# Performance work log

Measured on AMD Instinct MI355X. Metric: run time of the kernel, lower is better.

The kernel has to match this reference:

```python
import jax
import jax.numpy as jnp
from jax import lax
import numpy as np

# ---- static RPN config (mirrors init_kwargs) ----
STRIDES = (8, 16)
SIZES = ((32, 32), (16, 16))
SCALES = ((64.0 ** 2,), (128.0 ** 2,))
RATIOS = ((0.5, 1.0, 2.0), (0.5, 1.0, 2.0))
IMAGE_SIZE = (256, 256)
NMS_THRESH = 0.7
POST_NMS_TOP_N = 2000
NUM_LEVELS = 2
TOP_K_PER_LEVEL = POST_NMS_TOP_N // NUM_LEVELS  # padded NMS output slots per level


def _generate_anchors(stride, scales, ratios, size, image_size):
    """Anchors of shape (H*W*A, 4) in (x1,y1,x2,y2), clamped to image."""
    H, W = size
    cy = (np.arange(H, dtype=np.float32) + 0.5) * stride
    cx = (np.arange(W, dtype=np.float32) + 0.5) * stride
    ws, hs = [], []
    for s in scales:
        for r in ratios:
            ws.append(np.sqrt(s / r))
            hs.append(np.sqrt(s * r))
    ws = np.asarray(ws, np.float32)  # [A]
    hs = np.asarray(hs, np.float32)
    cxg, cyg = np.meshgrid(cx, cy)  # [H, W]
    x1 = cxg[..., None] - 0.5 * ws
    y1 = cyg[..., None] - 0.5 * hs
    x2 = cxg[..., None] + 0.5 * ws
    y2 = cyg[..., None] + 0.5 * hs
    a = np.stack([x1, y1, x2, y2], axis=-1)  # [H, W, A, 4]
    a[..., 0] = np.clip(a[..., 0], 0, image_size[0])
    a[..., 1] = np.clip(a[..., 1], 0, image_size[1])
    a[..., 2] = np.clip(a[..., 2], 0, image_size[0])
    a[..., 3] = np.clip(a[..., 3], 0, image_size[1])
    return a.reshape(-1, 4).astype(np.float32)


ANCHORS = [
    _generate_anchors(STRIDES[i], SCALES[i], RATIOS[i], SIZES[i], IMAGE_SIZE)
    for i in range(NUM_LEVELS)
]


def conv2d(x, w, b, padding):
    y = lax.conv_general_dilated(
        x, w, window_strides=(1, 1), padding=padding,
        dimension_numbers=("NCHW", "OIHW", "NCHW"))
    return y + b[None, :, None, None]


def decode_boxes(anchors, deltas):
    """Standard R-CNN box decode. anchors [N,4], deltas [..., N, 4]."""
    wa = anchors[:, 2] - anchors[:, 0]
    ha = anchors[:, 3] - anchors[:, 1]
    cxa = anchors[:, 0] + 0.5 * wa
    cya = anchors[:, 1] + 0.5 * ha
    dx, dy, dw, dh = deltas[..., 0], deltas[..., 1], deltas[..., 2], deltas[..., 3]
    cx = dx * wa + cxa
    cy = dy * ha + cya
    w = jnp.exp(dw) * wa
    h = jnp.exp(dh) * ha
    return jnp.stack([cx - 0.5 * w, cy - 0.5 * h, cx + 0.5 * w, cy + 0.5 * h], axis=-1)


def clamp_boxes(b):
    return jnp.stack([
        jnp.clip(b[..., 0], 0.0, IMAGE_SIZE[0]),
        jnp.clip(b[..., 1], 0.0, IMAGE_SIZE[1]),
        jnp.clip(b[..., 2], 0.0, IMAGE_SIZE[0]),
        jnp.clip(b[..., 3], 0.0, IMAGE_SIZE[1]),
    ], axis=-1)


def _pairwise_iou(b):
    # b: [N, 4] -> [N, N] IoU (torchvision convention, no +1)
    area = (b[:, 2] - b[:, 0]) * (b[:, 3] - b[:, 1])
    lt = jnp.maximum(b[:, None, :2], b[None, :, :2])
    rb = jnp.minimum(b[:, None, 2:], b[None, :, 2:])
    wh = jnp.clip(rb - lt, 0.0)
    inter = wh[..., 0] * wh[..., 1]
    return inter / (area[:, None] + area[None, :] - inter)


def nms_padded(boxes, scores, thresh, top_k):
    """Exact greedy NMS; returns (top_k,4) boxes and (top_k,) scores padded with -1."""
    N = boxes.shape[0]
    order = jnp.argsort(-scores)
    b = boxes[order]
    s = scores[order]
    iou = _pairwise_iou(b)  # [N, N]

    def body(supp, xs):
        row, i = xs
        keep_i = jnp.logical_not(supp[i])
        supp = supp | (keep_i & (row > thresh) & (jnp.arange(N) > i))
        return supp, keep_i

    _, keep = lax.scan(body, jnp.zeros((N,), bool), (iou, jnp.arange(N)))
    rank = jnp.cumsum(keep) - 1  # position among kept, in score order
    slot = jnp.where(keep & (rank < top_k), rank, top_k)  # overflow -> dump row
    out_b = jnp.full((top_k + 1, 4), -1.0, boxes.dtype).at[slot].set(b)
    out_s = jnp.full((top_k + 1,), -1.0, scores.dtype).at[slot].set(s)
    return out_b[:top_k], out_s[:top_k]


def _rpn_level(feat, anchors, conv_w, conv_b, cls_w, cls_b, reg_w, reg_b):
    x = jax.nn.relu(conv2d(feat, conv_w, conv_b, "SAME"))
    cls = conv2d(x, cls_w, cls_b, "VALID")              # [BS, A, H, W]
    reg = conv2d(x, reg_w, reg_b, "VALID")              # [BS, 4A, H, W]
    BS, A, H, W = cls.shape
    cls = cls.transpose(0, 2, 3, 1).reshape(BS, -1)                      # [BS, HWA]
    reg = reg.transpose(0, 2, 3, 1).reshape(BS, H, W, A, 4).reshape(BS, -1, 4)
    boxes = clamp_boxes(decode_boxes(anchors, lax.stop_gradient(reg)))   # [BS, HWA, 4]
    scores = jax.nn.sigmoid(lax.stop_gradient(cls))                      # [BS, HWA]
    kb, ks = jax.vmap(lambda bb, ss: nms_padded(bb, ss, NMS_THRESH, TOP_K_PER_LEVEL))(boxes, scores)
    return kb, ks


def setup_inputs() -> dict:
    key = jax.random.key(0)
    ks = jax.random.split(key, 5)
    C = 256
    A = 3
    return {
        "feat0": jax.random.normal(ks[0], (4, C, 32, 32), jnp.float32),
        "feat1": jax.random.normal(ks[1], (4, C, 16, 16), jnp.float32),
        "conv_w": 0.01 * jax.random.normal(ks[2], (C, C, 3, 3), jnp.float32),
        "conv_b": jnp.zeros((C,), jnp.float32),
        "cls_w": 0.01 * jax.random.normal(ks[3], (A, C, 1, 1), jnp.float32),
        "cls_b": jnp.zeros((A,), jnp.float32),
        "reg_w": 0.01 * jax.random.normal(ks[4], (4 * A, C, 1, 1), jnp.float32),
        "reg_b": jnp.zeros((4 * A,), jnp.float32),
    }


def reference(feat0, feat1, conv_w, conv_b, cls_w, cls_b, reg_w, reg_b):
    feats = [feat0, feat1]
    kb_all, ks_all = [], []
    for i in range(NUM_LEVELS):
        kb, ks = _rpn_level(feats[i], jnp.asarray(ANCHORS[i]),
                            conv_w, conv_b, cls_w, cls_b, reg_w, reg_b)
        kb_all.append(kb)
        ks_all.append(ks)
    bboxes = jnp.concatenate(kb_all, axis=1)   # [BS, POST_NMS_TOP_N, 4]
    scores = jnp.concatenate(ks_all, axis=1)   # [BS, POST_NMS_TOP_N]
    idx = jnp.argsort(-scores, axis=1)         # descending; -1 pads go last
    bboxes = jnp.take_along_axis(bboxes, idx[..., None], axis=1)
    return bboxes
```

## Files before the change

kernel.cpp:

```cpp
#include <hip/hip_runtime.h>
#include <math.h>


typedef double d4 __attribute__((ext_vector_type(4)));

__global__ __launch_bounds__(256, 4) void conv3_sk_u(
    const float* __restrict__ feat0, const float* __restrict__ feat1,
    const float* __restrict__ conv_w,
    double* __restrict__ part0, double* __restrict__ part1)
{
  __shared__ float Ald[2][16][72];
  __shared__ float Bld[2][16][72];
  const int t = threadIdx.x;
  const int bid = blockIdx.x;
  const float* feat;
  double* part;
  int oc_t, p_t, k_base, hw_sh, w_sh, H;
  if (bid < 1024) {
    int kc = bid >> 8;
    feat = feat0; part = part0 + (size_t)kc * 4096 * 256;
    oc_t = bid & 3; p_t = (bid >> 2) & 63;
    k_base = kc * 576; hw_sh = 10; w_sh = 5; H = 32;
  } else {
    int b2 = bid - 1024;
    int kc = b2 >> 6;
    feat = feat1; part = part1 + (size_t)kc * 1024 * 256;
    oc_t = b2 & 3; p_t = (b2 >> 2) & 15;
    k_base = kc * 576; hw_sh = 8; w_sh = 4; H = 16;
  }
  const int oc_base = oc_t * 64;
  const int p_base  = p_t * 64;
  const int wmask = H - 1, hwmask = (1 << hw_sh) - 1;
  const int skk = t >> 4;
  const int q4  = (t & 15) * 4;

  float a_r[4], b_r[4];
  auto load_tile = [&](int kt) {
    const int k0 = k_base + kt * 16;
    const float* wrow = conv_w + (size_t)(oc_base + q4) * 2304 + (k0 + skk);
#pragma unroll
    for (int u = 0; u < 4; ++u) a_r[u] = wrow[(size_t)u * 2304];
    int p = p_base + q4;
    int b = p >> hw_sh, pin = p & hwmask;
    int y = pin >> w_sh, x0 = pin & wmask;
    int k = k0 + skk;
    int ic = k / 9, rr = k - ic * 9;
    int ky = rr / 3, kx = rr - ky * 3;
    int iy = y + ky - 1;
    const float* frow = feat + (((b << 8) + ic) << hw_sh) + (iy << w_sh);
    bool yok = (unsigned)iy < (unsigned)H;
#pragma unroll
    for (int u = 0; u < 4; ++u) {
      int ix = x0 + u + kx - 1;
      b_r[u] = (yok && (unsigned)ix < (unsigned)H) ? frow[ix] : 0.f;
    }
  };

  const int lane = t & 63;
  const int wv = t >> 6;
  const int wo = (wv >> 1) << 5;
  const int wp = (wv & 1) << 5;
  const int lr = lane >> 4;
  const int lc = lane & 15;

  int rowm[4], colm[4];
  {
    d4 pz = {0.0, 0.0, 0.0, 0.0};
    double pa1 = (lr == 0) ? (double)(lc + 1) : 0.0;
    double pb1 = (lr == 0) ? 1.0 : 0.0;
    d4 prow = __builtin_amdgcn_mfma_f64_16x16x4f64(pa1, pb1, pz, 0, 0, 0);
    double pa2 = (lr == 0) ? 1.0 : 0.0;
    double pb2 = (lr == 0) ? (double)(lc + 1) : 0.0;
    d4 pcol = __builtin_amdgcn_mfma_f64_16x16x4f64(pa2, pb2, pz, 0, 0, 0);
#pragma unroll
    for (int d = 0; d < 4; ++d) {
      rowm[d] = ((int)prow[d] - 1) & 15;
      colm[d] = ((int)pcol[d] - 1) & 15;
    }
  }

  d4 acc00 = {0.0, 0.0, 0.0, 0.0};
  d4 acc01 = {0.0, 0.0, 0.0, 0.0};
  d4 acc10 = {0.0, 0.0, 0.0, 0.0};
  d4 acc11 = {0.0, 0.0, 0.0, 0.0};

  load_tile(0);
  for (int kt = 0; kt < 36; ++kt) {
    const int buf = kt & 1;
    *(float4*)&Ald[buf][skk][q4] = make_float4(a_r[0], a_r[1], a_r[2], a_r[3]);
    *(float4*)&Bld[buf][skk][q4] = make_float4(b_r[0], b_r[1], b_r[2], b_r[3]);
    __syncthreads();
    if (kt + 1 < 36) load_tile(kt + 1);
#pragma unroll
    for (int kc = 0; kc < 4; ++kc) {
      const int kr = (kc << 2) + lr;
      double a0 = (double)Ald[buf][kr][wo + lc];
      double a1 = (double)Ald[buf][kr][wo + 16 + lc];
      double b0 = (double)Bld[buf][kr][wp + lc];
      double b1 = (double)Bld[buf][kr][wp + 16 + lc];
      acc00 = __builtin_amdgcn_mfma_f64_16x16x4f64(a0, b0, acc00, 0, 0, 0);
      acc01 = __builtin_amdgcn_mfma_f64_16x16x4f64(a0, b1, acc01, 0, 0, 0);
      acc10 = __builtin_amdgcn_mfma_f64_16x16x4f64(a1, b0, acc10, 0, 0, 0);
      acc11 = __builtin_amdgcn_mfma_f64_16x16x4f64(a1, b1, acc11, 0, 0, 0);
    }
  }

  {
    const int p00 = p_base + wp;
    const int oc00 = oc_base + wo;
#pragma unroll
    for (int d = 0; d < 4; ++d) {
      const int rm = rowm[d], cm = colm[d];
      part[(size_t)(p00 + cm)      * 256 + (oc00 + rm)]      = acc00[d];
      part[(size_t)(p00 + 16 + cm) * 256 + (oc00 + rm)]      = acc01[d];
      part[(size_t)(p00 + cm)      * 256 + (oc00 + 16 + rm)] = acc10[d];
      part[(size_t)(p00 + 16 + cm) * 256 + (oc00 + 16 + rm)] = acc11[d];
    }
  }
}

__global__ __launch_bounds__(256) void rhd_k(
    const double* __restrict__ part0, const double* __restrict__ part1,
    const float* __restrict__ conv_b,
    const float* __restrict__ cls_w, const float* __restrict__ cls_b,
    const float* __restrict__ reg_w, const float* __restrict__ reg_b,
    float* __restrict__ box0, float* __restrict__ sc0,
    float* __restrict__ box1, float* __restrict__ sc1)
{
  int wid = (blockIdx.x * 256 + threadIdx.x) >> 6;
  int lane = threadIdx.x & 63;
  int lvl = wid >= 4096;
  const double* part = lvl ? part1 : part0;
  int p = lvl ? wid - 4096 : wid;
  int M = lvl ? 1024 : 4096;
  double s4[4];
  {
    float4 bv = ((const float4*)conv_b)[lane];
    s4[0] = (double)bv.x; s4[1] = (double)bv.y;
    s4[2] = (double)bv.z; s4[3] = (double)bv.w;
  }
#pragma unroll
  for (int ks = 0; ks < 4; ++ks) {
    const double2* pr = (const double2*)(part + (size_t)ks * M * 256 + (size_t)p * 256);
    double2 a = pr[2 * lane], b = pr[2 * lane + 1];
    s4[0] += a.x; s4[1] += a.y; s4[2] += b.x; s4[3] += b.y;
  }
  float xv[4];
#pragma unroll
  for (int q = 0; q < 4; ++q) {
    float f = (float)s4[q];
    xv[q] = f > 0.f ? f : 0.f;
  }
  double acc[15];
#pragma unroll
  for (int o = 0; o < 15; ++o) {
    const float* wr = (o < 3) ? (cls_w + o * 256) : (reg_w + (o - 3) * 256);
    float4 wv = ((const float4*)wr)[lane];
    acc[o] = (double)wv.x * (double)xv[0] + (double)wv.y * (double)xv[1] +
             (double)wv.z * (double)xv[2] + (double)wv.w * (double)xv[3];
  }
#pragma unroll
  for (int d = 1; d < 64; d <<= 1)
#pragma unroll
    for (int o = 0; o < 15; ++o)
      acc[o] += __shfl_xor(acc[o], d, 64);
  if (lane < 3) {
    int a = lane;
    float cls = (float)(acc[a] + (double)cls_b[a]);
    float score = 1.f / (1.f + expf(-cls));
    float dx = (float)(acc[3 + a * 4 + 0] + (double)reg_b[a * 4 + 0]);
    float dy = (float)(acc[3 + a * 4 + 1] + (double)reg_b[a * 4 + 1]);
    float dw = (float)(acc[3 + a * 4 + 2] + (double)reg_b[a * 4 + 2]);
    float dh = (float)(acc[3 + a * 4 + 3] + (double)reg_b[a * 4 + 3]);
    int hw_sh = lvl ? 8 : 10, w_sh = lvl ? 4 : 5, Wd = lvl ? 16 : 32;
    float S = lvl ? 16.f : 8.f;
    double scale = lvl ? 16384.0 : 4096.0;
    int b = p >> hw_sh, pin = p & ((1 << hw_sh) - 1);
    int y = pin >> w_sh, x = pin & (Wd - 1);
    double ratio = (a == 0) ? 0.5 : (a == 1 ? 1.0 : 2.0);
    float w_a = (float)sqrt(scale / ratio);
    float h_a = (float)sqrt(scale * ratio);
    float cx = ((float)x + 0.5f) * S;
    float cy = ((float)y + 0.5f) * S;
    float x1 = cx - 0.5f * w_a, y1 = cy - 0.5f * h_a;
    float x2 = cx + 0.5f * w_a, y2 = cy + 0.5f * h_a;
    x1 = fminf(fmaxf(x1, 0.f), 256.f); y1 = fminf(fmaxf(y1, 0.f), 256.f);
    x2 = fminf(fmaxf(x2, 0.f), 256.f); y2 = fminf(fmaxf(y2, 0.f), 256.f);
    float wa = x2 - x1, ha = y2 - y1;
    float cxa = x1 + 0.5f * wa, cya = y1 + 0.5f * ha;
    float ncx = dx * wa + cxa;
    float ncy = dy * ha + cya;
    float nw = expf(dw) * wa;
    float nh = expf(dh) * ha;
    float bx1 = ncx - 0.5f * nw, by1 = ncy - 0.5f * nh;
    float bx2 = ncx + 0.5f * nw, by2 = ncy + 0.5f * nh;
    bx1 = fminf(fmaxf(bx1, 0.f), 256.f); by1 = fminf(fmaxf(by1, 0.f), 256.f);
    bx2 = fminf(fmaxf(bx2, 0.f), 256.f); by2 = fminf(fmaxf(by2, 0.f), 256.f);
    int n = pin * 3 + a;
    if (lvl) {
      ((float4*)box1)[(size_t)b * 768 + n] = make_float4(bx1, by1, bx2, by2);
      sc1[b * 768 + n] = score;
    } else {
      ((float4*)box0)[(size_t)b * 3072 + n] = make_float4(bx1, by1, bx2, by2);
      sc0[b * 3072 + n] = score;
    }
  }
}

__global__ __launch_bounds__(256) void sort_level_k(
    const float* __restrict__ sc0, const float* __restrict__ box0,
    float* __restrict__ ssc0, float* __restrict__ sbox0,
    const float* __restrict__ sc1, const float* __restrict__ box1,
    float* __restrict__ ssc1, float* __restrict__ sbox1)
{
  __shared__ __align__(16) float s[3072];
  int z = blockIdx.x;
  const float *sc, *box; float *ssc, *sbox; int N, b, c;
  if (z < 48) { sc = sc0; box = box0; ssc = ssc0; sbox = sbox0; N = 3072; b = z / 12; c = z % 12; }
  else { int z2 = z - 48; sc = sc1; box = box1; ssc = ssc1; sbox = sbox1; N = 768; b = z2 / 3; c = z2 % 3; }
  const float* scb = sc + (size_t)b * N;
  for (int j = threadIdx.x; j < N; j += 256) s[j] = scb[j];
  __syncthreads();
  int i = c * 256 + threadIdx.x;
  float si = s[i];
  int rank = 0;
  const float4* sv = (const float4*)s;
  for (int j4 = 0; j4 < (N >> 2); ++j4) {
    float4 v = sv[j4];
    int j = j4 * 4;
    rank += (v.x > si) || (v.x == si && (j + 0) < i);
    rank += (v.y > si) || (v.y == si && (j + 1) < i);
    rank += (v.z > si) || (v.z == si && (j + 2) < i);
    rank += (v.w > si) || (v.w == si && (j + 3) < i);
  }
  ssc[(size_t)b * N + rank] = si;
  float4 bi = ((const float4*)box)[(size_t)b * N + i];
  ((float4*)sbox)[(size_t)b * N + rank] = bi;
}

__global__ __launch_bounds__(256) void mask_col_k(
    const float* __restrict__ sbox0, const float* __restrict__ sbox1,
    unsigned long long* __restrict__ mask0, unsigned long long* __restrict__ mask1,
    unsigned long long* __restrict__ colD0, unsigned long long* __restrict__ colD1)
{
  int bid = blockIdx.x;
  if (bid < 2448) {
    __shared__ float4 bj[64];
    const float* sbox; unsigned long long* mask; int N, words, w, i_ch, b;
    if (bid < 2304) {
      sbox = sbox0; mask = mask0; N = 3072; words = 48;
      w = bid % 48; int r = bid / 48; i_ch = r % 12; b = r / 12;
    } else {
      int z = bid - 2304;
      sbox = sbox1; mask = mask1; N = 768; words = 12;
      w = z % 12; int r = z / 12; i_ch = r % 3; b = r / 3;
    }
    int i = i_ch * 256 + threadIdx.x;
    if (threadIdx.x < 64)
      bj[threadIdx.x] = ((const float4*)sbox)[(size_t)b * N + w * 64 + threadIdx.x];
    __syncthreads();
    float4 bi = ((const float4*)sbox)[(size_t)b * N + i];
    float ai = (bi.z - bi.x) * (bi.w - bi.y);
    unsigned long long m = 0ull;
#pragma unroll 16
    for (int jj = 0; jj < 64; ++jj) {
      int j = w * 64 + jj;
      float4 bv = bj[jj];
      float lx = fmaxf(bi.x, bv.x), ly = fmaxf(bi.y, bv.y);
      float rx = fminf(bi.z, bv.z), ry = fminf(bi.w, bv.w);
      float iw = fmaxf(rx - lx, 0.f), ih = fmaxf(ry - ly, 0.f);
      float inter = iw * ih;
      float aj = (bv.z - bv.x) * (bv.w - bv.y);
      float iou = inter / (ai + aj - inter);
      if ((iou > 0.7f) & (j > i)) m |= (1ull << jj);
    }
    mask[((size_t)b * N + i) * words + w] = m;
  } else {
    __shared__ float4 tb[4][64];
    int sub = threadIdx.x >> 6, lane = threadIdx.x & 63;
    const float* sbox; unsigned long long* colD; int N, tile, b;
    if (bid < 2496) {
      int unit = (bid - 2448) * 4 + sub;
      sbox = sbox0; colD = colD0; N = 3072;
      tile = unit % 48; b = unit / 48;
    } else {
      int unit = (bid - 2496) * 4 + sub;
      sbox = sbox1; colD = colD1; N = 768;
      tile = unit % 12; b = unit / 12;
    }
    tb[sub][lane] = ((const float4*)sbox)[(size_t)b * N + tile * 64 + lane];
    __syncthreads();
    float4 bq = tb[sub][lane];
    float aq = (bq.z - bq.x) * (bq.w - bq.y);
    unsigned long long col = 0ull;
#pragma unroll 16
    for (int ii = 0; ii < 64; ++ii) {
      float4 bi = tb[sub][ii];
      float lx = fmaxf(bq.x, bi.x), ly = fmaxf(bq.y, bi.y);
      float rx = fminf(bq.z, bi.z), ry = fminf(bq.w, bi.w);
      float iw = fmaxf(rx - lx, 0.f), ih = fmaxf(ry - ly, 0.f);
      float inter = iw * ih;
      float ai = (bi.z - bi.x) * (bi.w - bi.y);
      float iou = inter / (aq + ai - inter);
      if ((iou > 0.7f) & (lane > ii)) col |= (1ull << ii);
    }
    colD[(size_t)b * N + tile * 64 + lane] = col;
  }
}

__global__ __launch_bounds__(256) void nms_scan_k(
    const float* __restrict__ ssc0, const float* __restrict__ sbox0,
    const unsigned long long* __restrict__ mask0,
    const unsigned long long* __restrict__ colD0,
    const float* __restrict__ ssc1, const float* __restrict__ sbox1,
    const unsigned long long* __restrict__ mask1,
    const unsigned long long* __restrict__ colD1,
    float* __restrict__ cb, float* __restrict__ cs)
{
  int z = blockIdx.x;
  int lvl = z >> 2, b = z & 3;
  int N = lvl ? 768 : 3072;
  int words = lvl ? 12 : 48;
  const float* ssc = (lvl ? ssc1 : ssc0) + (size_t)b * N;
  const float4* sbox = ((const float4*)(lvl ? sbox1 : sbox0)) + (size_t)b * N;
  const unsigned long long* mask = (lvl ? mask1 : mask0) + (size_t)b * N * words;
  const unsigned long long* colD = (lvl ? colD1 : colD0) + (size_t)b * N;
  const int tid = threadIdx.x;
  const int lane = tid & 63;
  const int wv = tid >> 6;
  float* csb = cs + (size_t)b * 2000 + lvl * 1000;
  float4* cbb = (float4*)(cb + ((size_t)b * 2000 + lvl * 1000) * 4);

  __shared__ unsigned long long rem[48];
  __shared__ unsigned long long part[4][64];
  __shared__ unsigned long long keepSh;
  __shared__ int doneSh;

  if (tid < 48) rem[tid] = 0ull;
  if (tid == 0) doneSh = 0;
  for (int q = tid; q < 1000; q += 256) {
    csb[q] = -1.f;
    cbb[q] = make_float4(-1.f, -1.f, -1.f, -1.f);
  }
  unsigned long long colv = 0ull; float sc_i = 0.f; float4 bx_i;
  if (wv == 0) { colv = colD[lane]; sc_i = ssc[lane]; bx_i = sbox[lane]; }
  int kept_base = 0;
  __syncthreads();

  for (int t = 0; t < words; ++t) {
    unsigned long long v[16];
    if (lane < words) {
      const unsigned long long* rowb =
          mask + ((size_t)t * 64 + wv * 16) * words + lane;
#pragma unroll
      for (int s = 0; s < 16; ++s) v[s] = rowb[(size_t)s * words];
    }
    if (wv == 0) {
      unsigned long long wr = rem[t];
      bool rm = (wr >> lane) & 1ull;
      bool kp = false;
      unsigned long long Rv = wr;
      unsigned long long Kv = 0ull;
      while (true) {
        bool F = (!rm) && (!kp) && ((colv & ~Rv) == 0ull);
        unsigned long long Fv = __ballot(F);
        if (Fv == 0ull) break;
        kp = kp || F;
        Kv |= Fv;
        bool newr = (!rm) && (!kp) && ((colv & Fv) != 0ull);
        rm = rm || newr;
        Rv = __ballot(rm);
      }
      if (kp) {
        int rank = kept_base + __popcll(Kv & ((1ull << lane) - 1ull));
        if (rank < 1000) { csb[rank] = sc_i; cbb[rank] = bx_i; }
      }
      kept_base += __popcll(Kv);
      if (lane == 0) {
        keepSh = Kv;
        doneSh = (kept_base >= 1000 || t + 1 >= words) ? 1 : 0;
      }
      if (t + 1 < words) {
        int i2 = (t + 1) * 64 + lane;
        colv = colD[i2]; sc_i = ssc[i2]; bx_i = sbox[i2];
      }
    }
    __syncthreads();
    unsigned long long k64 = keepSh;
    int done = doneSh;
    if (lane < words) {
      unsigned long long acc = 0ull;
#pragma unroll
      for (int s = 0; s < 16; ++s)
        acc |= (((k64 >> (wv * 16 + s)) & 1ull) ? v[s] : 0ull);
      part[wv][lane] = acc;
    }
    __syncthreads();
    if (done) break;
    if (tid > t && tid < words)
      rem[tid] |= part[0][tid] | part[1][tid] | part[2][tid] | part[3][tid];
    __syncthreads();
  }
}

__global__ __launch_bounds__(256) void final_sort_k(
    const float* __restrict__ cs, const float* __restrict__ cb,
    float* __restrict__ out)
{
  __shared__ __align__(16) float s[2000];
  int b = blockIdx.x >> 3, c = blockIdx.x & 7;
  const float* csb = cs + (size_t)b * 2000;
  for (int j = threadIdx.x; j < 2000; j += 256) s[j] = csb[j];
  __syncthreads();
  if (threadIdx.x >= 250) return;
  int li = c * 250 + threadIdx.x;
  float si = s[li];
  int rank = 0;
  const float4* sv = (const float4*)s;
  for (int j4 = 0; j4 < 500; ++j4) {
    float4 v = sv[j4];
    int j = j4 * 4;
    rank += (v.x > si) || (v.x == si && (j + 0) < li);
    rank += (v.y > si) || (v.y == si && (j + 1) < li);
    rank += (v.z > si) || (v.z == si && (j + 2) < li);
    rank += (v.w > si) || (v.w == si && (j + 3) < li);
  }
  float4 bi = ((const float4*)cb)[(size_t)b * 2000 + li];
  ((float4*)out)[(size_t)b * 2000 + rank] = bi;
}

extern "C" void kernel_launch(void* const* d_in, const int* in_sizes, int n_in,
                              void* d_out, int out_size, void* d_ws, size_t ws_size,
                              hipStream_t stream) {
  const float* feat0  = (const float*)d_in[0];
  const float* feat1  = (const float*)d_in[1];
  const float* conv_w = (const float*)d_in[2];
  const float* conv_b = (const float*)d_in[3];
  const float* cls_w  = (const float*)d_in[4];
  const float* cls_b  = (const float*)d_in[5];
  const float* reg_w  = (const float*)d_in[6];
  const float* reg_b  = (const float*)d_in[7];

  char* p = (char*)d_ws;
  auto alloc = [&](size_t bytes) {
    char* r = p;
    p += (bytes + 255) & ~(size_t)255;
    return r;
  };
  double* part0 = (double*)alloc((size_t)4 * 4096 * 256 * 8);
  double* part1 = (double*)alloc((size_t)4 * 1024 * 256 * 8);
  float* box0 = (float*)alloc((size_t)4 * 3072 * 16);
  float* sc0  = (float*)alloc((size_t)4 * 3072 * 4);
  float* box1 = (float*)alloc((size_t)4 * 768 * 16);
  float* sc1  = (float*)alloc((size_t)4 * 768 * 4);
  float* sbox0 = (float*)alloc((size_t)4 * 3072 * 16);
  float* ssc0  = (float*)alloc((size_t)4 * 3072 * 4);
  float* sbox1 = (float*)alloc((size_t)4 * 768 * 16);
  float* ssc1  = (float*)alloc((size_t)4 * 768 * 4);
  unsigned long long* mask0 = (unsigned long long*)alloc((size_t)4 * 3072 * 48 * 8);
  unsigned long long* mask1 = (unsigned long long*)alloc((size_t)4 * 768 * 12 * 8);
  unsigned long long* colD0 = (unsigned long long*)alloc((size_t)4 * 3072 * 8);
  unsigned long long* colD1 = (unsigned long long*)alloc((size_t)4 * 768 * 8);
  float* cb = (float*)alloc((size_t)4 * 2000 * 16);
  float* cs = (float*)alloc((size_t)4 * 2000 * 4);

  conv3_sk_u<<<1280, 256, 0, stream>>>(feat0, feat1, conv_w, part0, part1);
  rhd_k<<<1280, 256, 0, stream>>>(part0, part1, conv_b, cls_w, cls_b,
                                  reg_w, reg_b, box0, sc0, box1, sc1);
  sort_level_k<<<60, 256, 0, stream>>>(sc0, box0, ssc0, sbox0,
                                       sc1, box1, ssc1, sbox1);
  mask_col_k<<<2508, 256, 0, stream>>>(sbox0, sbox1, mask0, mask1, colD0, colD1);
  nms_scan_k<<<8, 256, 0, stream>>>(ssc0, sbox0, mask0, colD0,
                                    ssc1, sbox1, mask1, colD1, cb, cs);
  final_sort_k<<<32, 256, 0, stream>>>(cs, cb, (float*)d_out);
}
```

Baseline: 467.7 us.

## Fuse post-conv stages into one persistent kernel with grid-wide soft barriers

Replaces the five post-convolution kernels (head decode, per-level sort, IoU mask build, NMS scan, final sort) with a single persistent kernel of 512 blocks. The stages are separated by software grid barriers that use atomic counters, and a memset clears the counters before each run. The goal is to remove per-launch overhead and the gaps between the small, serial stages. The risks are deadlock if all 512 blocks are not co-resident, and the cost of spinning on the global atomics.

After: 674.4 us. 44.2% more time.

```diff
diff --git a/kernel.cpp b/kernel.cpp
--- a/kernel.cpp
+++ b/kernel.cpp
@@ -119,314 +119,322 @@
   }
 }
 
-__global__ __launch_bounds__(256) void rhd_k(
+__device__ __forceinline__ void soft_barrier(unsigned int* bar, int idx) {
+  __syncthreads();
+  if (threadIdx.x == 0) {
+    __threadfence();
+    atomicAdd(&bar[idx], 1u);
+    while (atomicAdd(&bar[idx], 0u) < 512u)
+      __builtin_amdgcn_s_sleep(8);
+    __threadfence();
+  }
+  __syncthreads();
+}
+
+__global__ __launch_bounds__(256, 4) void fused_post_k(
     const double* __restrict__ part0, const double* __restrict__ part1,
     const float* __restrict__ conv_b,
     const float* __restrict__ cls_w, const float* __restrict__ cls_b,
     const float* __restrict__ reg_w, const float* __restrict__ reg_b,
     float* __restrict__ box0, float* __restrict__ sc0,
-    float* __restrict__ box1, float* __restrict__ sc1)
+    float* __restrict__ box1, float* __restrict__ sc1,
+    float* __restrict__ sbox0, float* __restrict__ ssc0,
+    float* __restrict__ sbox1, float* __restrict__ ssc1,
+    unsigned long long* __restrict__ mask0, unsigned long long* __restrict__ mask1,
+    unsigned long long* __restrict__ colD0, unsigned long long* __restrict__ colD1,
+    float* __restrict__ cb, float* __restrict__ cs,
+    float* __restrict__ out, unsigned int* bar)
 {
-  int wid = (blockIdx.x * 256 + threadIdx.x) >> 6;
-  int lane = threadIdx.x & 63;
-  int lvl = wid >= 4096;
-  const double* part = lvl ? part1 : part0;
-  int p = lvl ? wid - 4096 : wid;
-  int M = lvl ? 1024 : 4096;
-  double s4[4];
-  {
-    float4 bv = ((const float4*)conv_b)[lane];
-    s4[0] = (double)bv.x; s4[1] = (double)bv.y;
-    s4[2] = (double)bv.z; s4[3] = (double)bv.w;
-  }
-#pragma unroll
-  for (int ks = 0; ks < 4; ++ks) {
-    const double2* pr = (const double2*)(part + (size_t)ks * M * 256 + (size_t)p * 256);
-    double2 a = pr[2 * lane], b = pr[2 * lane + 1];
-    s4[0] += a.x; s4[1] += a.y; s4[2] += b.x; s4[3] += b.y;
-  }
-  float xv[4];
-#pragma unroll
-  for (int q = 0; q < 4; ++q) {
-    float f = (float)s4[q];
-    xv[q] = f > 0.f ? f : 0.f;
-  }
-  double acc[15];
-#pragma unroll
-  for (int o = 0; o < 15; ++o) {
-    const float* wr = (o < 3) ? (cls_w + o * 256) : (reg_w + (o - 3) * 256);
-    float4 wv = ((const float4*)wr)[lane];
-    acc[o] = (double)wv.x * (double)xv[0] + (double)wv.y * (double)xv[1] +
-             (double)wv.z * (double)xv[2] + (double)wv.w * (double)xv[3];
-  }
-#pragma unroll
-  for (int d = 1; d < 64; d <<= 1)
-#pragma unroll
-    for (int o = 0; o < 15; ++o)
-      acc[o] += __shfl_xor(acc[o], d, 64);
-  if (lane < 3) {
-    int a = lane;
-    float cls = (float)(acc[a] + (double)cls_b[a]);
-    float score = 1.f / (1.f + expf(-cls));
-    float dx = (float)(acc[3 + a * 4 + 0] + (double)reg_b[a * 4 + 0]);
-    float dy = (float)(acc[3 + a * 4 + 1] + (double)reg_b[a * 4 + 1]);
-    float dw = (float)(acc[3 + a * 4 + 2] + (double)reg_b[a * 4 + 2]);
-    float dh = (float)(acc[3 + a * 4 + 3] + (double)reg_b[a * 4 + 3]);
-    int hw_sh = lvl ? 8 : 10, w_sh = lvl ? 4 : 5, Wd = lvl ? 16 : 32;
-    float S = lvl ? 16.f : 8.f;
-    double scale = lvl ? 16384.0 : 4096.0;
-    int b = p >> hw_sh, pin = p & ((1 << hw_sh) - 1);
-    int y = pin >> w_sh, x = pin & (Wd - 1);
-    double ratio = (a == 0) ? 0.5 : (a == 1 ? 1.0 : 2.0);
-    float w_a = (float)sqrt(scale / ratio);
-    float h_a = (float)sqrt(scale * ratio);
-    float cx = ((float)x + 0.5f) * S;
-    float cy = ((float)y + 0.5f) * S;
-    float x1 = cx - 0.5f * w_a, y1 = cy - 0.5f * h_a;
-    float x2 = cx + 0.5f * w_a, y2 = cy + 0.5f * h_a;
-    x1 = fminf(fmaxf(x1, 0.f), 256.f); y1 = fminf(fmaxf(y1, 0.f), 256.f);
-    x2 = fminf(fmaxf(x2, 0.f), 256.f); y2 = fminf(fmaxf(y2, 0.f), 256.f);
-    float wa = x2 - x1, ha = y2 - y1;
-    float cxa = x1 + 0.5f * wa, cya = y1 + 0.5f * ha;
-    float ncx = dx * wa + cxa;
-    float ncy = dy * ha + cya;
-    float nw = expf(dw) * wa;
-    float nh = expf(dh) * ha;
-    float bx1 = ncx - 0.5f * nw, by1 = ncy - 0.5f * nh;
-    float bx2 = ncx + 0.5f * nw, by2 = ncy + 0.5f * nh;
-    bx1 = fminf(fmaxf(bx1, 0.f), 256.f); by1 = fminf(fmaxf(by1, 0.f), 256.f);
-    bx2 = fminf(fmaxf(bx2, 0.f), 256.f); by2 = fminf(fmaxf(by2, 0.f), 256.f);
-    int n = pin * 3 + a;
-    if (lvl) {
-      ((float4*)box1)[(size_t)b * 768 + n] = make_float4(bx1, by1, bx2, by2);
-      sc1[b * 768 + n] = score;
+  __shared__ __align__(16) char smem[12288];
+  const int t = threadIdx.x;
+
+  for (int u = blockIdx.x; u < 1280; u += 512) {
+    int wid = (u * 256 + t) >> 6;
+    int lane = t & 63;
+    int lvl = wid >= 4096;
+    const double* part = lvl ? part1 : part0;
+    int p = lvl ? wid - 4096 : wid;
+    int M = lvl ? 1024 : 4096;
+    double s4[4];
+    {
+      float4 bv = ((const float4*)conv_b)[lane];
+      s4[0] = (double)bv.x; s4[1] = (double)bv.y;
+      s4[2] = (double)bv.z; s4[3] = (double)bv.w;
+    }
+#pragma unroll
+    for (int ks = 0; ks < 4; ++ks) {
+      const double2* pr = (const double2*)(part + (size_t)ks * M * 256 + (size_t)p * 256);
+      double2 a = pr[2 * lane], b = pr[2 * lane + 1];
+      s4[0] += a.x; s4[1] += a.y; s4[2] += b.x; s4[3] += b.y;
+    }
+    float xv[4];
+#pragma unroll
+    for (int q = 0; q < 4; ++q) {
+      float f = (float)s4[q];
+      xv[q] = f > 0.f ? f : 0.f;
+    }
+    double acc[15];
+#pragma unroll
+    for (int o = 0; o < 15; ++o) {
+      const float* wr = (o < 3) ? (cls_w + o * 256) : (reg_w + (o - 3) * 256);
+      float4 wv = ((const float4*)wr)[lane];
+      acc[o] = (double)wv.x * (double)xv[0] + (double)wv.y * (double)xv[1] +
+               (double)wv.z * (double)xv[2] + (double)wv.w * (double)xv[3];
+    }
+#pragma unroll
+    for (int d = 1; d < 64; d <<= 1)
+#pragma unroll
+      for (int o = 0; o < 15; ++o)
+        acc[o] += __shfl_xor(acc[o], d, 64);
+    if (lane < 3) {
+      int a = lane;
+      float cls = (float)(acc[a] + (double)cls_b[a]);
+      float score = 1.f / (1.f + expf(-cls));
+      float dx = (float)(acc[3 + a * 4 + 0] + (double)reg_b[a * 4 + 0]);
+      float dy = (float)(acc[3 + a * 4 + 1] + (double)reg_b[a * 4 + 1]);
+      float dw = (float)(acc[3 + a * 4 + 2] + (double)reg_b[a * 4 + 2]);
+      float dh = (float)(acc[3 + a * 4 + 3] + (double)reg_b[a * 4 + 3]);
+      int hw_sh = lvl ? 8 : 10, w_sh = lvl ? 4 : 5, Wd = lvl ? 16 : 32;
+      float S = lvl ? 16.f : 8.f;
+      double scale = lvl ? 16384.0 : 4096.0;
+      int b = p >> hw_sh, pin = p & ((1 << hw_sh) - 1);
+      int y = pin >> w_sh, x = pin & (Wd - 1);
+      double ratio = (a == 0) ? 0.5 : (a == 1 ? 1.0 : 2.0);
+      float w_a = (float)sqrt(scale / ratio);
+      float h_a = (float)sqrt(scale * ratio);
+      float cx = ((float)x + 0.5f) * S;
+      float cy = ((float)y + 0.5f) * S;
+      float x1 = cx - 0.5f * w_a, y1 = cy - 0.5f * h_a;
+      float x2 = cx + 0.5f * w_a, y2 = cy + 0.5f * h_a;
+      x1 = fminf(fmaxf(x1, 0.f), 256.f); y1 = fminf(fmaxf(y1, 0.f), 256.f);
+      x2 = fminf(fmaxf(x2, 0.f), 256.f); y2 = fminf(fmaxf(y2, 0.f), 256.f);
+      float wa = x2 - x1, ha = y2 - y1;
+      float cxa = x1 + 0.5f * wa, cya = y1 + 0.5f * ha;
+      float ncx = dx * wa + cxa;
+      float ncy = dy * ha + cya;
+      float nw = expf(dw) * wa;
+      float nh = expf(dh) * ha;
+      float bx1 = ncx - 0.5f * nw, by1 = ncy - 0.5f * nh;
+      float bx2 = ncx + 0.5f * nw, by2 = ncy + 0.5f * nh;
+      bx1 = fminf(fmaxf(bx1, 0.f), 256.f); by1 = fminf(fmaxf(by1, 0.f), 256.f);
+      bx2 = fminf(fmaxf(bx2, 0.f), 256.f); by2 = fminf(fmaxf(by2, 0.f), 256.f);
+      int n = pin * 3 + a;
+      if (lvl) {
+        ((float4*)box1)[(size_t)b * 768 + n] = make_float4(bx1, by1, bx2, by2);
+        sc1[b * 768 + n] = score;
+      } else {
+        ((float4*)box0)[(size_t)b * 3072 + n] = make_float4(bx1, by1, bx2, by2);
+        sc0[b * 3072 + n] = score;
+      }
+    }
+  }
+  soft_barrier(bar, 0);
+
+  if (blockIdx.x < 60) {
+    float* s = (float*)smem;
+    int z = blockIdx.x;
+    const float *sc, *box; float *ssc, *sbox; int N, b, c;
+    if (z < 48) { sc = sc0; box = box0; ssc = ssc0; sbox = sbox0; N = 3072; b = z / 12; c = z % 12; }
+    else { int z2 = z - 48; sc = sc1; box = box1; ssc = ssc1; sbox = sbox1; N = 768; b = z2 / 3; c = z2 % 3; }
+    const float* scb = sc + (size_t)b * N;
+    for (int j = t; j < N; j += 256) s[j] = scb[j];
+    __syncthreads();
+    int i = c * 256 + t;
+    float si = s[i];
+    int rank = 0;
+    const float4* sv = (const float4*)s;
+    for (int j4 = 0; j4 < (N >> 2); ++j4) {
+      float4 v = sv[j4];
+      int j = j4 * 4;
+      rank += (v.x > si) || (v.x == si && (j + 0) < i);
+      rank += (v.y > si) || (v.y == si && (j + 1) < i);
+      rank += (v.z > si) || (v.z == si && (j + 2) < i);
+      rank += (v.w > si) || (v.w == si && (j + 3) < i);
+    }
+    ssc[(size_t)b * N + rank] = si;
+    float4 bi = ((const float4*)box)[(size_t)b * N + i];
+    ((float4*)sbox)[(size_t)b * N + rank] = bi;
+  }
+  soft_barrier(bar, 1);
+
+  for (int bid = blockIdx.x; bid < 2508; bid += 512) {
+    if (bid < 2448) {
+      float4* bj = (float4*)smem;
+      const float* sbox; unsigned long long* mask; int N, words, w, i_ch, b;
+      if (bid < 2304) {
+        sbox = sbox0; mask = mask0; N = 3072; words = 48;
+        w = bid % 48; int r = bid / 48; i_ch = r % 12; b = r / 12;
+      } else {
+        int z = bid - 2304;
+        sbox = sbox1; mask = mask1; N = 768; words = 12;
+        w = z % 12; int r = z / 12; i_ch = r % 3; b = r / 3;
+      }
+      int i = i_ch * 256 + t;
+      if (t < 64)
+        bj[t] = ((const float4*)sbox)[(size_t)b * N + w * 64 + t];
+      __syncthreads();
+      float4 bi = ((const float4*)sbox)[(size_t)b * N + i];
+      float ai = (bi.z - bi.x) * (bi.w - bi.y);
+      unsigned long long m = 0ull;
+#pragma unroll 16
+      for (int jj = 0; jj < 64; ++jj) {
+        int j = w * 64 + jj;
+        float4 bv = bj[jj];
+        float lx = fmaxf(bi.x, bv.x), ly = fmaxf(bi.y, bv.y);
+        float rx = fminf(bi.z, bv.z), ry = fminf(bi.w, bv.w);
+        float iw = fmaxf(rx - lx, 0.f), ih = fmaxf(ry - ly, 0.f);
+        float inter = iw * ih;
+        float aj = (bv.z - bv.x) * (bv.w - bv.y);
+        float iou = inter / (ai + aj - inter);
+        if ((iou > 0.7f) & (j > i)) m |= (1ull << jj);
+      }
+      mask[((size_t)b * N + i) * words + w] = m;
     } else {
-      ((float4*)box0)[(size_t)b * 3072 + n] = make_float4(bx1, by1, bx2, by2);
-      sc0[b * 3072 + n] = score;
-    }
-  }
-}
-
-__global__ __launch_bounds__(256) void sort_level_k(
-    const float* __restrict__ sc0, const float* __restrict__ box0,
-    float* __restrict__ ssc0, float* __restrict__ sbox0,
-    const float* __restrict__ sc1, const float* __restrict__ box1,
-    float* __restrict__ ssc1, float* __restrict__ sbox1)
-{
-  __shared__ __align__(16) float s[3072];
-  int z = blockIdx.x;
-  const float *sc, *box; float *ssc, *sbox; int N, b, c;
-  if (z < 48) { sc = sc0; box = box0; ssc = ssc0; sbox = sbox0; N = 3072; b = z / 12; c = z % 12; }
-  else { int z2 = z - 48; sc = sc1; box = box1; ssc = ssc1; sbox = sbox1; N = 768; b = z2 / 3; c = z2 % 3; }
-  const float* scb = sc + (size_t)b * N;
-  for (int j = threadIdx.x; j < N; j += 256) s[j] = scb[j];
-  __syncthreads();
-  int i = c * 256 + threadIdx.x;
-  float si = s[i];
-  int rank = 0;
-  const float4* sv = (const float4*)s;
-  for (int j4 = 0; j4 < (N >> 2); ++j4) {
-    float4 v = sv[j4];
-    int j = j4 * 4;
-    rank += (v.x > si) || (v.x == si && (j + 0) < i);
-    rank += (v.y > si) || (v.y == si && (j + 1) < i);
-    rank += (v.z > si) || (v.z == si && (j + 2) < i);
-    rank += (v.w > si) || (v.w == si && (j + 3) < i);
-  }
-  ssc[(size_t)b * N + rank] = si;
-  float4 bi = ((const float4*)box)[(size_t)b * N + i];
-  ((float4*)sbox)[(size_t)b * N + rank] = bi;
-}
-
-__global__ __launch_bounds__(256) void mask_col_k(
-    const float* __restrict__ sbox0, const float* __restrict__ sbox1,
-    unsigned long long* __restrict__ mask0, unsigned long long* __restrict__ mask1,
-    unsigned long long* __restrict__ colD0, unsigned long long* __restrict__ colD1)
-{
-  int bid = blockIdx.x;
-  if (bid < 2448) {
-    __shared__ float4 bj[64];
-    const float* sbox; unsigned long long* mask; int N, words, w, i_ch, b;
-    if (bid < 2304) {
-      sbox = sbox0; mask = mask0; N = 3072; words = 48;
-      w = bid % 48; int r = bid / 48; i_ch = r % 12; b = r / 12;
-    } else {
-      int z = bid - 2304;
-      sbox = sbox1; mask = mask1; N = 768; words = 12;
-      w = z % 12; int r = z / 12; i_ch = r % 3; b = r / 3;
-    }
-    int i = i_ch * 256 + threadIdx.x;
-    if (threadIdx.x < 64)
-      bj[threadIdx.x] = ((const float4*)sbox)[(size_t)b * N + w * 64 + threadIdx.x];
+      float4 (*tb)[64] = (float4(*)[64])smem;
+      int sub = t >> 6, lane = t & 63;
+      const float* sbox; unsigned long long* colD; int N, tile, b;
+      if (bid < 2496) {
+        int unit = (bid - 2448) * 4 + sub;
+        sbox = sbox0; colD = colD0; N = 3072;
+        tile = unit % 48; b = unit / 48;
+      } else {
+        int unit = (bid - 2496) * 4 + sub;
+        sbox = sbox1; colD = colD1; N = 768;
+        tile = unit % 12; b = unit / 12;
+      }
+      tb[sub][lane] = ((const float4*)sbox)[(size_t)b * N + tile * 64 + lane];
+      __syncthreads();
+      float4 bq = tb[sub][lane];
+      float aq = (bq.z - bq.x) * (bq.w - bq.y);
+      unsigned long long col = 0ull;
+#pragma unroll 16
+      for (int ii = 0; ii < 64; ++ii) {
+        float4 bi = tb[sub][ii];
+        float lx = fmaxf(bq.x, bi.x), ly = fmaxf(bq.y, bi.y);
+        float rx = fminf(bq.z, bi.z), ry = fminf(bq.w, bi.w);
+        float iw = fmaxf(rx - lx, 0.f), ih = fmaxf(ry - ly, 0.f);
+        float inter = iw * ih;
+        float ai = (bi.z - bi.x) * (bi.w - bi.y);
+        float iou = inter / (aq + ai - inter);
+        if ((iou > 0.7f) & (lane > ii)) col |= (1ull << ii);
+      }
+      colD[(size_t)b * N + tile * 64 + lane] = col;
+    }
     __syncthreads();
-    float4 bi = ((const float4*)sbox)[(size_t)b * N + i];
-    float ai = (bi.z - bi.x) * (bi.w - bi.y);
-    unsigned long long m = 0ull;
-#pragma unroll 16
-    for (int jj = 0; jj < 64; ++jj) {
-      int j = w * 64 + jj;
-      float4 bv = bj[jj];
-      float lx = fmaxf(bi.x, bv.x), ly = fmaxf(bi.y, bv.y);
-      float rx = fminf(bi.z, bv.z), ry = fminf(bi.w, bv.w);
-      float iw = fmaxf(rx - lx, 0.f), ih = fmaxf(ry - ly, 0.f);
-      float inter = iw * ih;
-      float aj = (bv.z - bv.x) * (bv.w - bv.y);
-      float iou = inter / (ai + aj - inter);
-      if ((iou > 0.7f) & (j > i)) m |= (1ull << jj);
-    }
-    mask[((size_t)b * N + i) * words + w] = m;
-  } else {
-    __shared__ float4 tb[4][64];
-    int sub = threadIdx.x >> 6, lane = threadIdx.x & 63;
-    const float* sbox; unsigned long long* colD; int N, tile, b;
-    if (bid < 2496) {
-      int unit = (bid - 2448) * 4 + sub;
-      sbox = sbox0; colD = colD0; N = 3072;
-      tile = unit % 48; b = unit / 48;
-    } else {
-      int unit = (bid - 2496) * 4 + sub;
-      sbox = sbox1; colD = colD1; N = 768;
-      tile = unit % 12; b = unit / 12;
-    }
-    tb[sub][lane] = ((const float4*)sbox)[(size_t)b * N + tile * 64 + lane];
+  }
+  soft_barrier(bar, 2);
+
+  if (blockIdx.x < 8) {
+    int z = blockIdx.x;
+    int lvl = z >> 2, b = z & 3;
+    int N = lvl ? 768 : 3072;
+    int words = lvl ? 12 : 48;
+    const float* ssc = (lvl ? ssc1 : ssc0) + (size_t)b * N;
+    const float4* sbox = ((const float4*)(lvl ? sbox1 : sbox0)) + (size_t)b * N;
+    const unsigned long long* mask = (lvl ? mask1 : mask0) + (size_t)b * N * words;
+    const unsigned long long* colD = (lvl ? colD1 : colD0) + (size_t)b * N;
+    const int lane = t & 63;
+    const int wv = t >> 6;
+    float* csb = cs + (size_t)b * 2000 + lvl * 1000;
+    float4* cbb = (float4*)(cb + ((size_t)b * 2000 + lvl * 1000) * 4);
+
+    unsigned long long* rem = (unsigned long long*)smem;
+    unsigned long long (*npart)[64] =
+        (unsigned long long(*)[64])(smem + 384);
+    unsigned long long* keepShp = (unsigned long long*)(smem + 384 + 2048);
+    int* doneShp = (int*)(smem + 384 + 2048 + 8);
+
+    if (t < 48) rem[t] = 0ull;
+    if (t == 0) *doneShp = 0;
+    for (int q = t; q < 1000; q += 256) {
+      csb[q] = -1.f;
+      cbb[q] = make_float4(-1.f, -1.f, -1.f, -1.f);
+    }
+    unsigned long long colv = 0ull; float sc_i = 0.f; float4 bx_i;
+    if (wv == 0) { colv = colD[lane]; sc_i = ssc[lane]; bx_i = sbox[lane]; }
+    int kept_base = 0;
     __syncthreads();
-    float4 bq = tb[sub][lane];
-    float aq = (bq.z - bq.x) * (bq.w - bq.y);
-    unsigned long long col = 0ull;
-#pragma unroll 16
-    for (int ii = 0; ii < 64; ++ii) {
-      float4 bi = tb[sub][ii];
-      float lx = fmaxf(bq.x, bi.x), ly = fmaxf(bq.y, bi.y);
-      float rx = fminf(bq.z, bi.z), ry = fminf(bq.w, bi.w);
-      float iw = fmaxf(rx - lx, 0.f), ih = fmaxf(ry - ly, 0.f);
-      float inter = iw * ih;
-      float ai = (bi.z - bi.x) * (bi.w - bi.y);
-      float iou = inter / (aq + ai - inter);
-      if ((iou > 0.7f) & (lane > ii)) col |= (1ull << ii);
-    }
-    colD[(size_t)b * N + tile * 64 + lane] = col;
-  }
-}
-
-__global__ __launch_bounds__(256) void nms_scan_k(
-    const float* __restrict__ ssc0, const float* __restrict__ sbox0,
-    const unsigned long long* __restrict__ mask0,
-    const unsigned long long* __restrict__ colD0,
-    const float* __restrict__ ssc1, const float* __restrict__ sbox1,
-    const unsigned long long* __restrict__ mask1,
-    const unsigned long long* __restrict__ colD1,
-    float* __restrict__ cb, float* __restrict__ cs)
-{
-  int z = blockIdx.x;
-  int lvl = z >> 2, b = z & 3;
-  int N = lvl ? 768 : 3072;
-  int words = lvl ? 12 : 48;
-  const float* ssc = (lvl ? ssc1 : ssc0) + (size_t)b * N;
-  const float4* sbox = ((const float4*)(lvl ? sbox1 : sbox0)) + (size_t)b * N;
-  const unsigned long long* mask = (lvl ? mask1 : mask0) + (size_t)b * N * words;
-  const unsigned long long* colD = (lvl ? colD1 : colD0) + (size_t)b * N;
-  const int tid = threadIdx.x;
-  const int lane = tid & 63;
-  const int wv = tid >> 6;
-  float* csb = cs + (size_t)b * 2000 + lvl * 1000;
-  float4* cbb = (float4*)(cb + ((size_t)b * 2000 + lvl * 1000) * 4);
-
-  __shared__ unsigned long long rem[48];
-  __shared__ unsigned long long part[4][64];
-  __shared__ unsigned long long keepSh;
-  __shared__ int doneSh;
-
-  if (tid < 48) rem[tid] = 0ull;
-  if (tid == 0) doneSh = 0;
-  for (int q = tid; q < 1000; q += 256) {
-    csb[q] = -1.f;
-    cbb[q] = make_float4(-1.f, -1.f, -1.f, -1.f);
-  }
-  unsigned long long colv = 0ull; float sc_i = 0.f; float4 bx_i;
-  if (wv == 0) { colv = colD[lane]; sc_i = ssc[lane]; bx_i = sbox[lane]; }
-  int kept_base = 0;
-  __syncthreads();
-
-  for (int t = 0; t < words; ++t) {
-    unsigned long long v[16];
-    if (lane < words) {
-      const unsigned long long* rowb =
-          mask + ((size_t)t * 64 + wv * 16) * words + lane;
-#pragma unroll
-      for (int s = 0; s < 16; ++s) v[s] = rowb[(size_t)s * words];
-    }
-    if (wv == 0) {
-      unsigned long long wr = rem[t];
-      bool rm = (wr >> lane) & 1ull;
-      bool kp = false;
-      unsigned long long Rv = wr;
-      unsigned long long Kv = 0ull;
-      while (true) {
-        bool F = (!rm) && (!kp) && ((colv & ~Rv) == 0ull);
-        unsigned long long Fv = __ballot(F);
-        if (Fv == 0ull) break;
-        kp = kp || F;
-        Kv |= Fv;
-        bool newr = (!rm) && (!kp) && ((colv & Fv) != 0ull);
-        rm = rm || newr;
-        Rv = __ballot(rm);
-      }
-      if (kp) {
-        int rank = kept_base + __popcll(Kv & ((1ull << lane) - 1ull));
-        if (rank < 1000) { csb[rank] = sc_i; cbb[rank] = bx_i; }
-      }
-      kept_base += __popcll(Kv);
-      if (lane == 0) {
-        keepSh = Kv;
-        doneSh = (kept_base >= 1000 || t + 1 >= words) ? 1 : 0;
-      }
-      if (t + 1 < words) {
-        int i2 = (t + 1) * 64 + lane;
-        colv = colD[i2]; sc_i = ssc[i2]; bx_i = sbox[i2];
-      }
-    }
+
+    for (int tt = 0; tt < words; ++tt) {
+      unsigned long long v[16];
+      if (lane < words) {
+        const unsigned long long* rowb =
+            mask + ((size_t)tt * 64 + wv * 16) * words + lane;
+#pragma unroll
+        for (int s = 0; s < 16; ++s) v[s] = rowb[(size_t)s * words];
+      }
+      if (wv == 0) {
+        unsigned long long wr = rem[tt];
+        bool rm = (wr >> lane) & 1ull;
+        bool kp = false;
+        unsigned long long Rv = wr;
+        unsigned long long Kv = 0ull;
+        while (true) {
+          bool F = (!rm) && (!kp) && ((colv & ~Rv) == 0ull);
+          unsigned long long Fv = __ballot(F);
+          if (Fv == 0ull) break;
+          kp = kp || F;
+          Kv |= Fv;
+          bool newr = (!rm) && (!kp) && ((colv & Fv) != 0ull);
+          rm = rm || newr;
+          Rv = __ballot(rm);
+        }
+        if (kp) {
+          int rank = kept_base + __popcll(Kv & ((1ull << lane) - 1ull));
+          if (rank < 1000) { csb[rank] = sc_i; cbb[rank] = bx_i; }
+        }
+        kept_base += __popcll(Kv);
+        if (lane == 0) {
+          *keepShp = Kv;
+          *doneShp = (kept_base >= 1000 || tt + 1 >= words) ? 1 : 0;
+        }
+        if (tt + 1 < words) {
+          int i2 = (tt + 1) * 64 + lane;
+          colv = colD[i2]; sc_i = ssc[i2]; bx_i = sbox[i2];
+        }
+      }
+      __syncthreads();
+      unsigned long long k64 = *keepShp;
+      int done = *doneShp;
+      if (lane < words) {
+        unsigned long long acc = 0ull;
+#pragma unroll
+        for (int s = 0; s < 16; ++s)
+          acc |= (((k64 >> (wv * 16 + s)) & 1ull) ? v[s] : 0ull);
+        npart[wv][lane] = acc;
+      }
+      __syncthreads();
+      if (done) break;
+      if (t > tt && t < words)
+        rem[t] |= npart[0][t] | npart[1][t] | npart[2][t] | npart[3][t];
+      __syncthreads();
+    }
+  }
+  soft_barrier(bar, 3);
+
+  if (blockIdx.x < 32) {
+    float* s = (float*)smem;
+    int b = blockIdx.x >> 3, c = blockIdx.x & 7;
+    const float* csb = cs + (size_t)b * 2000;
+    for (int j = t; j < 2000; j += 256) s[j] = csb[j];
     __syncthreads();
-    unsigned long long k64 = keepSh;
-    int done = doneSh;
-    if (lane < words) {
-      unsigned long long acc = 0ull;
-#pragma unroll
-      for (int s = 0; s < 16; ++s)
-        acc |= (((k64 >> (wv * 16 + s)) & 1ull) ? v[s] : 0ull);
-      part[wv][lane] = acc;
-    }
-    __syncthreads();
-    if (done) break;
-    if (tid > t && tid < words)
-      rem[tid] |= part[0][tid] | part[1][tid] | part[2][tid] | part[3][tid];
-    __syncthreads();
-  }
-}
-
-__global__ __launch_bounds__(256) void final_sort_k(
-    const float* __restrict__ cs, const float* __restrict__ cb,
-    float* __restrict__ out)
-{
-  __shared__ __align__(16) float s[2000];
-  int b = blockIdx.x >> 3, c = blockIdx.x & 7;
-  const float* csb = cs + (size_t)b * 2000;
-  for (int j = threadIdx.x; j < 2000; j += 256) s[j] = csb[j];
-  __syncthreads();
-  if (threadIdx.x >= 250) return;
-  int li = c * 250 + threadIdx.x;
-  float si = s[li];
-  int rank = 0;
-  const float4* sv = (const float4*)s;
-  for (int j4 = 0; j4 < 500; ++j4) {
-    float4 v = sv[j4];
-    int j = j4 * 4;
-    rank += (v.x > si) || (v.x == si && (j + 0) < li);
-    rank += (v.y > si) || (v.y == si && (j + 1) < li);
-    rank += (v.z > si) || (v.z == si && (j + 2) < li);
-    rank += (v.w > si) || (v.w == si && (j + 3) < li);
-  }
-  float4 bi = ((const float4*)cb)[(size_t)b * 2000 + li];
-  ((float4*)out)[(size_t)b * 2000 + rank] = bi;
+    if (t < 250) {
+      int li = c * 250 + t;
+      float si = s[li];
+      int rank = 0;
+      const float4* sv = (const float4*)s;
+      for (int j4 = 0; j4 < 500; ++j4) {
+        float4 v = sv[j4];
+        int j = j4 * 4;
+        rank += (v.x > si) || (v.x == si && (j + 0) < li);
+        rank += (v.y > si) || (v.y == si && (j + 1) < li);
+        rank += (v.z > si) || (v.z == si && (j + 2) < li);
+        rank += (v.w > si) || (v.w == si && (j + 3) < li);
+      }
+      float4 bi = ((const float4*)cb)[(size_t)b * 2000 + li];
+      ((float4*)out)[(size_t)b * 2000 + rank] = bi;
+    }
+  }
 }
 
 extern "C" void kernel_launch(void* const* d_in, const int* in_sizes, int n_in,
@@ -463,14 +471,13 @@
   unsigned long long* colD1 = (unsigned long long*)alloc((size_t)4 * 768 * 8);
   float* cb = (float*)alloc((size_t)4 * 2000 * 16);
   float* cs = (float*)alloc((size_t)4 * 2000 * 4);
-
+  unsigned int* bar = (unsigned int*)alloc(256);
+  float* outp = (float*)d_out;
+
+  hipMemsetAsync(bar, 0, 256, stream);
   conv3_sk_u<<<1280, 256, 0, stream>>>(feat0, feat1, conv_w, part0, part1);
-  rhd_k<<<1280, 256, 0, stream>>>(part0, part1, conv_b, cls_w, cls_b,
-                                  reg_w, reg_b, box0, sc0, box1, sc1);
-  sort_level_k<<<60, 256, 0, stream>>>(sc0, box0, ssc0, sbox0,
-                                       sc1, box1, ssc1, sbox1);
-  mask_col_k<<<2508, 256, 0, stream>>>(sbox0, sbox1, mask0, mask1, colD0, colD1);
-  nms_scan_k<<<8, 256, 0, stream>>>(ssc0, sbox0, mask0, colD0,
-                                    ssc1, sbox1, mask1, colD1, cb, cs);
-  final_sort_k<<<32, 256, 0, stream>>>(cs, cb, (float*)d_out);
+  fused_post_k<<<512, 256, 0, stream>>>(
+      part0, part1, conv_b, cls_w, cls_b, reg_w, reg_b,
+      box0, sc0, box1, sc1, sbox0, ssc0, sbox1, ssc1,
+      mask0, mask1, colD0, colD1, cb, cs, outp, bar);
 }
```
